# Kernel tuning notes

Measured on AMD Instinct MI355X. Metric: run time of the kernel, lower is better.

Reference implementation:

```python
import jax, jax.numpy as jnp
import numpy as np

NC = 13   # num_classes
NA = 5    # num_anchors
COORD_SCALE = 1.0
NOOBJECT_SCALE = 0.1
CLASS_SCALE = 1.0


def setup_inputs() -> dict:
    key = jax.random.key(0)
    k1, k2, k3 = jax.random.split(key, 3)
    nB, nH, nW = 32, 76, 76
    output = jax.random.normal(k1, (nB, NA * (19 + NC), nH, nW), dtype=jnp.float32)
    # target: channel 0 = class id (0 == background), channels 1..18 = nine (gx,gy)
    # keypoint coordinates in grid units.
    cls_t = jax.random.randint(k2, (nB, NA, nH, nW, 1), 0, NC).astype(jnp.float32)
    coords_t = jax.random.uniform(k3, (nB, NA, nH, nW, 18), dtype=jnp.float32) * nW
    target = jnp.concatenate([cls_t, coords_t], axis=-1)
    return {"output": output, "target": target}


def _region_loss(output, target):
    nB, nH, nW = output.shape[0], output.shape[2], output.shape[3]
    out = output.reshape(nB, NA, 19 + NC, nH, nW)
    cls_logits = out[:, :, :NC]          # [B,A,C,H,W]
    conf = out[:, :, NC]                 # [B,A,H,W] (raw, no sigmoid in source)
    coords = out[:, :, NC + 1:]          # [B,A,18,H,W]
    xs = coords[:, :, 0::2]              # [B,A,9,H,W]
    ys = coords[:, :, 1::2]
    # only the first keypoint (x0,y0) is passed through sigmoid in the source
    xs = jnp.concatenate([jax.nn.sigmoid(xs[:, :, :1]), xs[:, :, 1:]], axis=2)
    ys = jnp.concatenate([jax.nn.sigmoid(ys[:, :, :1]), ys[:, :, 1:]], axis=2)

    grid_x = jnp.arange(nW, dtype=output.dtype)             # broadcasts on W
    grid_y = jnp.arange(nH, dtype=output.dtype)[:, None]    # broadcasts on H

    # ground-truth keypoints -> cell-relative offsets (tx = gx - w, ty = gy - h)
    g = target[..., 1:].reshape(nB, NA, nH, nW, 9, 2)
    gx = jnp.transpose(g[..., 0], (0, 1, 4, 2, 3))          # [B,A,9,H,W]
    gy = jnp.transpose(g[..., 1], (0, 1, 4, 2, 3))
    txs = gx - grid_x
    tys = gy - grid_y

    # pred_boxes were built from .data in torch -> detached
    pxs = jax.lax.stop_gradient(xs + grid_x)
    pys = jax.lax.stop_gradient(ys + grid_y)

    # compute_conf: exp(2 - d/15) if d < 30 else 0, averaged over the 9 points
    dt = jnp.sqrt((txs - pxs) ** 2 + (tys - pys) ** 2)
    tconf = jnp.where(dt < 30.0, jnp.exp(2.0 - dt / 15.0), 0.0).mean(axis=2)

    obj = target[..., 0] != 0                                # [B,A,H,W]
    coor_mask = obj.astype(output.dtype)[:, :, None]         # [B,A,1,H,W]

    # coordinate loss: sum over 9 keypoints of MSE(x*m, tx*m)/2 (sum reduction)
    loss_coord = 0.5 * COORD_SCALE * (
        jnp.sum((coor_mask * (xs - txs)) ** 2)
        + jnp.sum((coor_mask * (ys - tys)) ** 2)
    )

    # confidence loss; conf_mask is uniformly noobject_scale in the source
    loss_conf = 0.5 * jnp.sum((NOOBJECT_SCALE * (conf - tconf)) ** 2)

    # class loss: sum-reduced cross entropy over object cells
    logp = jax.nn.log_softmax(cls_logits, axis=2)            # [B,A,C,H,W]
    tcls = target[..., 0].astype(jnp.int32)                  # [B,A,H,W]
    nll = -jnp.take_along_axis(logp, tcls[:, :, None], axis=2)[:, :, 0]
    loss_cls = CLASS_SCALE * jnp.sum(jnp.where(obj, nll, 0.0))

    return loss_coord + loss_conf + loss_cls


def reference(output, target):
    return _region_loss(output, target)
```

## Files before the change

### kernel.cpp

```cpp
#include <hip/hip_runtime.h>


namespace {

constexpr int kNC = 13;
constexpr int kCh = 32;
constexpr int kH = 76, kW = 76;
constexpr int kSP = kH * kW;
constexpr int kCells = 32 * 5 * kSP;
constexpr int kTPB = 512;
constexpr int kBlocks = kCells / kTPB;
constexpr int kTW = kTPB * 19;
constexpr int kF4 = kTW / 4;

__device__ __forceinline__ void gl16(const float* g, float* l) {
  __builtin_amdgcn_global_load_lds(
      (const __attribute__((address_space(1))) void*)g,
      (__attribute__((address_space(3))) void*)l, 16, 0, 0);
}

__global__ __launch_bounds__(512, 8)
void region_loss_v8(const float* __restrict__ out,
                    const float* __restrict__ tgt,
                    double* __restrict__ acc)
{
  __shared__ __align__(16) float tl[kTW];
  __shared__ float wsum[8];

  const int tid  = threadIdx.x;
  const int blk  = blockIdx.x;
  const int lane = tid & 63;
  const int w    = tid >> 6;

  const int n = blk * kTPB + tid;
  const int q = n / kSP;
  const int s = n - q * kSP;
  const float* op = out + (size_t)q * kCh * kSP + s;

  float ch[kCh];
#pragma unroll
  for (int c = 0; c < kCh; ++c) ch[c] = op[(size_t)c * kSP];

  const float* tg = tgt + (size_t)blk * kTW;
#pragma unroll
  for (int k = 0; k < 5; ++k) {
    const int i4 = (k * 8 + w) * 64;
    if (i4 < kF4)
      gl16(tg + (size_t)(i4 + lane) * 4, &tl[(size_t)i4 * 4]);
  }

  asm volatile("" :
      "+v"(ch[0]), "+v"(ch[1]), "+v"(ch[2]), "+v"(ch[3]),
      "+v"(ch[4]), "+v"(ch[5]), "+v"(ch[6]), "+v"(ch[7]),
      "+v"(ch[8]), "+v"(ch[9]), "+v"(ch[10]), "+v"(ch[11]),
      "+v"(ch[12]), "+v"(ch[13]), "+v"(ch[14]), "+v"(ch[15]));
  asm volatile("" :
      "+v"(ch[16]), "+v"(ch[17]), "+v"(ch[18]), "+v"(ch[19]),
      "+v"(ch[20]), "+v"(ch[21]), "+v"(ch[22]), "+v"(ch[23]),
      "+v"(ch[24]), "+v"(ch[25]), "+v"(ch[26]), "+v"(ch[27]),
      "+v"(ch[28]), "+v"(ch[29]), "+v"(ch[30]), "+v"(ch[31]));

  __syncthreads();

  const int hh = s / kW;
  const float fh = (float)hh;
  const float fw = (float)(s - hh * kW);

  const int rb = tid * 19;
  const float clsf = tl[rb];
  const bool obj = (clsf != 0.f);

  float tcf = 0.f, lcd = 0.f;
#pragma unroll
  for (int i = 0; i < 9; ++i) {
    float xv = ch[14 + 2 * i];
    float yv = ch[15 + 2 * i];
    if (i == 0) {
      xv = __builtin_amdgcn_rcpf(1.f + __expf(-xv));
      yv = __builtin_amdgcn_rcpf(1.f + __expf(-yv));
    }
    const float gx = tl[rb + 1 + 2 * i];
    const float gy = tl[rb + 2 + 2 * i];
    const float tx = gx - fw;
    const float ty = gy - fh;
    const float dx = tx - (xv + fw);
    const float dy = ty - (yv + fh);
    const float dt = sqrtf(dx * dx + dy * dy);
    if (dt < 30.f) tcf += __expf(2.f - dt * (1.f / 15.f));
    const float ex = xv - tx;
    const float ey = yv - ty;
    lcd += ex * ex + ey * ey;
  }

  const float d = ch[kNC] - tcf * (1.f / 9.f);
  float loss = 0.005f * d * d;
  if (obj) loss += 0.5f * lcd;

  if (obj) {
    float mx = ch[0];
#pragma unroll
    for (int c = 1; c < kNC; ++c) mx = fmaxf(mx, ch[c]);
    float se = 0.f;
#pragma unroll
    for (int c = 0; c < kNC; ++c) se += __expf(ch[c] - mx);
    const int tc = (int)clsf;
    float sel = 0.f;
#pragma unroll
    for (int c = 0; c < kNC; ++c) sel += (c == tc) ? ch[c] : 0.f;
    loss += -(sel - mx - __logf(se));
  }

#pragma unroll
  for (int off = 32; off > 0; off >>= 1)
    loss += __shfl_down(loss, off, 64);

  if (lane == 0) wsum[w] = loss;
  __syncthreads();
  if (tid == 0) {
    float b = 0.f;
#pragma unroll
    for (int i = 0; i < 8; ++i) b += wsum[i];
    atomicAdd(&acc[(blk & 63) * 8], (double)b);
  }
}

__global__ void finalize_kernel(const double* __restrict__ acc,
                                float* __restrict__ outv)
{
  const int lane = threadIdx.x;
  double v = acc[lane * 8];
#pragma unroll
  for (int off = 32; off > 0; off >>= 1)
    v += __shfl_down(v, off, 64);
  if (lane == 0) outv[0] = (float)v;
}

}

extern "C" void kernel_launch(void* const* d_in, const int* in_sizes, int n_in,
                              void* d_out, int out_size, void* d_ws, size_t ws_size,
                              hipStream_t stream) {
  const float* output = (const float*)d_in[0];
  const float* target = (const float*)d_in[1];
  double* acc = (double*)d_ws;

  hipMemsetAsync(acc, 0, 64 * 8 * sizeof(double), stream);

  region_loss_v8<<<kBlocks, kTPB, 0, stream>>>(output, target, acc);
  finalize_kernel<<<1, 64, 0, stream>>>(acc, (float*)d_out);
}
```

Baseline: 41.50 us.

## Use persistent grid with double-buffered slab prefetch into registers and LDS

Replaces the one-cell-per-thread launch with a persistent grid of 1024 blocks of 256 threads. Each block walks over 256-cell slabs and issues the next slab's 32 channel loads and its target LDS copy before computing the current slab, using explicit vmcnt waits. Each wave now loads only its own part of the target tile, which removes the block-wide barrier per slab. The goal is to overlap memory latency with compute in a memory-bound kernel. In exchange it doubles register pressure (two 32-float channel arrays) and relies on hand-counted vmcnt values that must match the number of loads issued.

```diff
diff --git a/kernel.cpp b/kernel.cpp
--- a/kernel.cpp
+++ b/kernel.cpp
@@ -8,10 +8,11 @@
 constexpr int kH = 76, kW = 76;
 constexpr int kSP = kH * kW;
 constexpr int kCells = 32 * 5 * kSP;
-constexpr int kTPB = 512;
-constexpr int kBlocks = kCells / kTPB;
-constexpr int kTW = kTPB * 19;
-constexpr int kF4 = kTW / 4;
+constexpr int kCPS = 256;
+constexpr int kSlabs = kCells / kCPS;
+constexpr int kGrid = 1024;
+constexpr int kWW = 64 * 19;
+constexpr int kTW = kCPS * 19;
 
 __device__ __forceinline__ void gl16(const float* g, float* l) {
   __builtin_amdgcn_global_load_lds(
@@ -19,36 +20,18 @@
       (__attribute__((address_space(3))) void*)l, 16, 0, 0);
 }
 
-__global__ __launch_bounds__(512, 8)
-void region_loss_v8(const float* __restrict__ out,
-                    const float* __restrict__ tgt,
-                    double* __restrict__ acc)
-{
-  __shared__ __align__(16) float tl[kTW];
-  __shared__ float wsum[8];
-
-  const int tid  = threadIdx.x;
-  const int blk  = blockIdx.x;
-  const int lane = tid & 63;
-  const int w    = tid >> 6;
-
-  const int n = blk * kTPB + tid;
+__device__ __forceinline__ void issueSlab(int slab, int tid, int lane, int w,
+                                          const float* __restrict__ out,
+                                          const float* __restrict__ tgt,
+                                          float* __restrict__ buf,
+                                          float ch[kCh])
+{
+  const int n = slab * kCPS + tid;
   const int q = n / kSP;
   const int s = n - q * kSP;
   const float* op = out + (size_t)q * kCh * kSP + s;
-
-  float ch[kCh];
 #pragma unroll
   for (int c = 0; c < kCh; ++c) ch[c] = op[(size_t)c * kSP];
-
-  const float* tg = tgt + (size_t)blk * kTW;
-#pragma unroll
-  for (int k = 0; k < 5; ++k) {
-    const int i4 = (k * 8 + w) * 64;
-    if (i4 < kF4)
-      gl16(tg + (size_t)(i4 + lane) * 4, &tl[(size_t)i4 * 4]);
-  }
-
   asm volatile("" :
       "+v"(ch[0]), "+v"(ch[1]), "+v"(ch[2]), "+v"(ch[3]),
       "+v"(ch[4]), "+v"(ch[5]), "+v"(ch[6]), "+v"(ch[7]),
@@ -60,8 +43,33 @@
       "+v"(ch[24]), "+v"(ch[25]), "+v"(ch[26]), "+v"(ch[27]),
       "+v"(ch[28]), "+v"(ch[29]), "+v"(ch[30]), "+v"(ch[31]));
 
-  __syncthreads();
-
+  const float* tg = tgt + (size_t)slab * kTW + w * kWW;
+  float* lb = buf + w * kWW;
+#pragma unroll
+  for (int k = 0; k < 4; ++k)
+    gl16(tg + (size_t)(k * 64 + lane) * 4, lb + k * 256);
+  if (lane < 48)
+    gl16(tg + (size_t)(256 + lane) * 4, lb + 1024);
+}
+
+#define WAIT_PREV() do {                                   \
+    __builtin_amdgcn_sched_barrier(0);                     \
+    asm volatile("s_waitcnt vmcnt(37)" ::: "memory");      \
+    __builtin_amdgcn_sched_barrier(0);                     \
+  } while (0)
+#define WAIT_ALL() do {                                    \
+    __builtin_amdgcn_sched_barrier(0);                     \
+    asm volatile("s_waitcnt vmcnt(0)" ::: "memory");       \
+    __builtin_amdgcn_sched_barrier(0);                     \
+  } while (0)
+
+__device__ __forceinline__ float computeSlab(int slab, int tid,
+                                             const float ch[kCh],
+                                             const float* __restrict__ tl)
+{
+  const int n = slab * kCPS + tid;
+  const int q = n / kSP;
+  const int s = n - q * kSP;
   const int hh = s / kW;
   const float fh = (float)hh;
   const float fw = (float)(s - hh * kW);
@@ -109,6 +117,51 @@
     for (int c = 0; c < kNC; ++c) sel += (c == tc) ? ch[c] : 0.f;
     loss += -(sel - mx - __logf(se));
   }
+  return loss;
+}
+
+__global__ __launch_bounds__(256, 4)
+void region_loss_v9(const float* __restrict__ out,
+                    const float* __restrict__ tgt,
+                    double* __restrict__ acc)
+{
+  __shared__ __align__(16) float buf0[kTW];
+  __shared__ __align__(16) float buf1[kTW];
+  __shared__ float wsum[4];
+
+  const int tid  = threadIdx.x;
+  const int lane = tid & 63;
+  const int w    = tid >> 6;
+
+  float chA[kCh], chB[kCh];
+  float loss = 0.f;
+
+  int t = blockIdx.x;
+  issueSlab(t, tid, lane, w, out, tgt, buf0, chA);
+
+  for (;;) {
+    const int t1 = t + kGrid;
+    if (t1 < kSlabs) {
+      issueSlab(t1, tid, lane, w, out, tgt, buf1, chB);
+      WAIT_PREV();
+      loss += computeSlab(t, tid, chA, buf0);
+      const int t2 = t1 + kGrid;
+      if (t2 < kSlabs) {
+        issueSlab(t2, tid, lane, w, out, tgt, buf0, chA);
+        WAIT_PREV();
+        loss += computeSlab(t1, tid, chB, buf1);
+        t = t2;
+      } else {
+        WAIT_ALL();
+        loss += computeSlab(t1, tid, chB, buf1);
+        break;
+      }
+    } else {
+      WAIT_ALL();
+      loss += computeSlab(t, tid, chA, buf0);
+      break;
+    }
+  }
 
 #pragma unroll
   for (int off = 32; off > 0; off >>= 1)
@@ -117,10 +170,8 @@
   if (lane == 0) wsum[w] = loss;
   __syncthreads();
   if (tid == 0) {
-    float b = 0.f;
-#pragma unroll
-    for (int i = 0; i < 8; ++i) b += wsum[i];
-    atomicAdd(&acc[(blk & 63) * 8], (double)b);
+    const float b = wsum[0] + wsum[1] + wsum[2] + wsum[3];
+    atomicAdd(&acc[(blockIdx.x & 63) * 8], (double)b);
   }
 }
 
@@ -146,6 +197,6 @@
 
   hipMemsetAsync(acc, 0, 64 * 8 * sizeof(double), stream);
 
-  region_loss_v8<<<kBlocks, kTPB, 0, stream>>>(output, target, acc);
+  region_loss_v9<<<kGrid, 256, 0, stream>>>(output, target, acc);
   finalize_kernel<<<1, 64, 0, stream>>>(acc, (float*)d_out);
 }
```

New measurement: 43.47 us. +4.8%, slower.

## Per-wave target staging, drop block barrier and finalize kernel

Applied to the files above, without the earlier changes.

Each wave now loads into LDS only the target slice for its own 64 cells, so a wave-local s_waitcnt vmcnt(0) replaces the block-wide __syncthreads before compute. The 64-slot double accumulators and the separate finalize kernel are removed; each block atomically adds its float partial straight into the output, which is zeroed by a memset. This cuts one kernel launch and a barrier stall, in exchange for float atomics contending on a single address and a summation order that is no longer deterministic.

```diff
diff --git a/kernel.cpp b/kernel.cpp
--- a/kernel.cpp
+++ b/kernel.cpp
@@ -10,8 +10,8 @@
 constexpr int kCells = 32 * 5 * kSP;
 constexpr int kTPB = 512;
 constexpr int kBlocks = kCells / kTPB;
+constexpr int kWW = 64 * 19;
 constexpr int kTW = kTPB * 19;
-constexpr int kF4 = kTW / 4;
 
 __device__ __forceinline__ void gl16(const float* g, float* l) {
   __builtin_amdgcn_global_load_lds(
@@ -20,9 +20,9 @@
 }
 
 __global__ __launch_bounds__(512, 8)
-void region_loss_v8(const float* __restrict__ out,
-                    const float* __restrict__ tgt,
-                    double* __restrict__ acc)
+void region_loss_v10(const float* __restrict__ out,
+                     const float* __restrict__ tgt,
+                     float* __restrict__ result)
 {
   __shared__ __align__(16) float tl[kTW];
   __shared__ float wsum[8];
@@ -41,13 +41,13 @@
 #pragma unroll
   for (int c = 0; c < kCh; ++c) ch[c] = op[(size_t)c * kSP];
 
-  const float* tg = tgt + (size_t)blk * kTW;
+  const float* tg = tgt + (size_t)blk * kTW + w * kWW;
+  float* lb = &tl[w * kWW];
 #pragma unroll
-  for (int k = 0; k < 5; ++k) {
-    const int i4 = (k * 8 + w) * 64;
-    if (i4 < kF4)
-      gl16(tg + (size_t)(i4 + lane) * 4, &tl[(size_t)i4 * 4]);
-  }
+  for (int k = 0; k < 4; ++k)
+    gl16(tg + (size_t)(k * 64 + lane) * 4, lb + k * 256);
+  if (lane < 48)
+    gl16(tg + (size_t)(256 + lane) * 4, lb + 1024);
 
   asm volatile("" :
       "+v"(ch[0]), "+v"(ch[1]), "+v"(ch[2]), "+v"(ch[3]),
@@ -60,7 +60,9 @@
       "+v"(ch[24]), "+v"(ch[25]), "+v"(ch[26]), "+v"(ch[27]),
       "+v"(ch[28]), "+v"(ch[29]), "+v"(ch[30]), "+v"(ch[31]));
 
-  __syncthreads();
+  __builtin_amdgcn_sched_barrier(0);
+  asm volatile("s_waitcnt vmcnt(0)" ::: "memory");
+  __builtin_amdgcn_sched_barrier(0);
 
   const int hh = s / kW;
   const float fh = (float)hh;
@@ -120,19 +122,8 @@
     float b = 0.f;
 #pragma unroll
     for (int i = 0; i < 8; ++i) b += wsum[i];
-    atomicAdd(&acc[(blk & 63) * 8], (double)b);
+    atomicAdd(result, b);
   }
-}
-
-__global__ void finalize_kernel(const double* __restrict__ acc,
-                                float* __restrict__ outv)
-{
-  const int lane = threadIdx.x;
-  double v = acc[lane * 8];
-#pragma unroll
-  for (int off = 32; off > 0; off >>= 1)
-    v += __shfl_down(v, off, 64);
-  if (lane == 0) outv[0] = (float)v;
 }
 
 }
@@ -142,10 +133,9 @@
                               hipStream_t stream) {
   const float* output = (const float*)d_in[0];
   const float* target = (const float*)d_in[1];
-  double* acc = (double*)d_ws;
+  float* result = (float*)d_out;
 
-  hipMemsetAsync(acc, 0, 64 * 8 * sizeof(double), stream);
+  hipMemsetAsync(result, 0, sizeof(float), stream);
 
-  region_loss_v8<<<kBlocks, kTPB, 0, stream>>>(output, target, acc);
-  finalize_kernel<<<1, 64, 0, stream>>>(acc, (float*)d_out);
+  region_loss_v10<<<kBlocks, kTPB, 0, stream>>>(output, target, result);
 }
```

New measurement: 46.83 us. 12.8% more time.

## Give each wave a private LDS slice and drop block-wide barriers

Applied to the files above, without the earlier changes.

Each 64-lane wave now stages its own target rows into a private LDS slice and waits only on its own vmcnt, with no __syncthreads before compute. The grid becomes a fixed 2048 blocks of 256 threads. Each wave handles one unit of 64 cells and, where one exists, a second unit 8192 units later, reusing the same LDS slice. This removes block-level sync stalls and amortises launch and reduction cost. The risk is that the second unit's loads are serialised behind the first, and the tail is uneven because only some waves get a second unit.

```diff
diff --git a/kernel.cpp b/kernel.cpp
--- a/kernel.cpp
+++ b/kernel.cpp
@@ -8,10 +8,9 @@
 constexpr int kH = 76, kW = 76;
 constexpr int kSP = kH * kW;
 constexpr int kCells = 32 * 5 * kSP;
-constexpr int kTPB = 512;
-constexpr int kBlocks = kCells / kTPB;
-constexpr int kTW = kTPB * 19;
-constexpr int kF4 = kTW / 4;
+constexpr int kUnits = kCells / 64;
+constexpr int kGrid  = 2048;
+constexpr int kWW = 64 * 19;
 
 __device__ __forceinline__ void gl16(const float* g, float* l) {
   __builtin_amdgcn_global_load_lds(
@@ -19,20 +18,12 @@
       (__attribute__((address_space(3))) void*)l, 16, 0, 0);
 }
 
-__global__ __launch_bounds__(512, 8)
-void region_loss_v8(const float* __restrict__ out,
-                    const float* __restrict__ tgt,
-                    double* __restrict__ acc)
+__device__ __forceinline__ float unitLoss(int u, int lane,
+                                          const float* __restrict__ out,
+                                          const float* __restrict__ tgt,
+                                          float* __restrict__ lb)
 {
-  __shared__ __align__(16) float tl[kTW];
-  __shared__ float wsum[8];
-
-  const int tid  = threadIdx.x;
-  const int blk  = blockIdx.x;
-  const int lane = tid & 63;
-  const int w    = tid >> 6;
-
-  const int n = blk * kTPB + tid;
+  const int n = u * 64 + lane;
   const int q = n / kSP;
   const int s = n - q * kSP;
   const float* op = out + (size_t)q * kCh * kSP + s;
@@ -41,13 +32,12 @@
 #pragma unroll
   for (int c = 0; c < kCh; ++c) ch[c] = op[(size_t)c * kSP];
 
-  const float* tg = tgt + (size_t)blk * kTW;
+  const float* tg = tgt + (size_t)u * kWW;
 #pragma unroll
-  for (int k = 0; k < 5; ++k) {
-    const int i4 = (k * 8 + w) * 64;
-    if (i4 < kF4)
-      gl16(tg + (size_t)(i4 + lane) * 4, &tl[(size_t)i4 * 4]);
-  }
+  for (int k = 0; k < 4; ++k)
+    gl16(tg + (size_t)(k * 64 + lane) * 4, lb + k * 256);
+  if (lane < 48)
+    gl16(tg + (size_t)(256 + lane) * 4, lb + 1024);
 
   asm volatile("" :
       "+v"(ch[0]), "+v"(ch[1]), "+v"(ch[2]), "+v"(ch[3]),
@@ -60,14 +50,16 @@
       "+v"(ch[24]), "+v"(ch[25]), "+v"(ch[26]), "+v"(ch[27]),
       "+v"(ch[28]), "+v"(ch[29]), "+v"(ch[30]), "+v"(ch[31]));
 
-  __syncthreads();
+  __builtin_amdgcn_sched_barrier(0);
+  asm volatile("s_waitcnt vmcnt(0)" ::: "memory");
+  __builtin_amdgcn_sched_barrier(0);
 
   const int hh = s / kW;
   const float fh = (float)hh;
   const float fw = (float)(s - hh * kW);
 
-  const int rb = tid * 19;
-  const float clsf = tl[rb];
+  const int rb = lane * 19;
+  const float clsf = lb[rb];
   const bool obj = (clsf != 0.f);
 
   float tcf = 0.f, lcd = 0.f;
@@ -79,8 +71,8 @@
       xv = __builtin_amdgcn_rcpf(1.f + __expf(-xv));
       yv = __builtin_amdgcn_rcpf(1.f + __expf(-yv));
     }
-    const float gx = tl[rb + 1 + 2 * i];
-    const float gy = tl[rb + 2 + 2 * i];
+    const float gx = lb[rb + 1 + 2 * i];
+    const float gy = lb[rb + 2 + 2 * i];
     const float tx = gx - fw;
     const float ty = gy - fh;
     const float dx = tx - (xv + fw);
@@ -109,6 +101,32 @@
     for (int c = 0; c < kNC; ++c) sel += (c == tc) ? ch[c] : 0.f;
     loss += -(sel - mx - __logf(se));
   }
+  return loss;
+}
+
+__global__ __launch_bounds__(256, 8)
+void region_loss_v11(const float* __restrict__ out,
+                     const float* __restrict__ tgt,
+                     double* __restrict__ acc)
+{
+  __shared__ __align__(16) float tl[4 * kWW];
+  __shared__ float wsum[4];
+
+  const int tid  = threadIdx.x;
+  const int lane = tid & 63;
+  const int w    = tid >> 6;
+  float* lb = &tl[w * kWW];
+
+  const int g = blockIdx.x * 4 + w;
+
+  float loss = unitLoss(g, lane, out, tgt, lb);
+
+  const int u1 = g + 8192;
+  if (u1 < kUnits) {
+    asm volatile("s_waitcnt lgkmcnt(0)" ::: "memory");
+    __builtin_amdgcn_sched_barrier(0);
+    loss += unitLoss(u1, lane, out, tgt, lb);
+  }
 
 #pragma unroll
   for (int off = 32; off > 0; off >>= 1)
@@ -117,10 +135,8 @@
   if (lane == 0) wsum[w] = loss;
   __syncthreads();
   if (tid == 0) {
-    float b = 0.f;
-#pragma unroll
-    for (int i = 0; i < 8; ++i) b += wsum[i];
-    atomicAdd(&acc[(blk & 63) * 8], (double)b);
+    const float b = wsum[0] + wsum[1] + wsum[2] + wsum[3];
+    atomicAdd(&acc[(blockIdx.x & 63) * 8], (double)b);
   }
 }
 
@@ -146,6 +162,6 @@
 
   hipMemsetAsync(acc, 0, 64 * 8 * sizeof(double), stream);
 
-  region_loss_v8<<<kBlocks, kTPB, 0, stream>>>(output, target, acc);
+  region_loss_v11<<<kGrid, 256, 0, stream>>>(output, target, acc);
   finalize_kernel<<<1, 64, 0, stream>>>(acc, (float*)d_out);
 }
```

After: 45.94 us. +10.7%, slower.
